# Kernel tuning notes

Hardware: AMD Instinct MI355X
Metric: run time of the kernel (lower is better)

## Reference

```python
import jax, jax.numpy as jnp
import numpy as np

B, N, D_IN, D_OUT, E = 2, 50000, 128, 64, 800000
NEG_SLOPE = 0.2  # LeakyReLU negative slope (alpha)


def setup_inputs() -> dict:
    key = jax.random.key(0)
    ks = jax.random.split(key, 8)
    X_key = jax.random.normal(ks[0], (B, N, D_IN), dtype=jnp.float32)
    X_value = jax.random.normal(ks[1], (B, N, D_IN), dtype=jnp.float32)
    src = jax.random.randint(ks[2], (E,), 0, N, dtype=jnp.int32)
    dst = jnp.sort(jax.random.randint(ks[3], (E,), 0, N, dtype=jnp.int32))
    s = 1.0 / np.sqrt(D_IN)
    Wk = jax.random.normal(ks[4], (D_IN, D_OUT), dtype=jnp.float32) * s
    bk = jnp.zeros((D_OUT,), dtype=jnp.float32)
    Wv = jax.random.normal(ks[5], (D_IN, D_OUT), dtype=jnp.float32) * s
    bv = jnp.zeros((D_OUT,), dtype=jnp.float32)
    return {"X_key": X_key, "X_value": X_value, "Wk": Wk, "bk": bk,
            "Wv": Wv, "bv": bv, "src": src, "dst": dst}


def reference(X_key, X_value, Wk, bk, Wv, bv, src, dst):
    n = X_key.shape[1]
    h_key = X_key @ Wk + bk      # [B, N, D_OUT]
    h_value = X_value @ Wv + bv  # [B, N, D_OUT]

    def per_batch(hk, hv):
        # per-edge dot-product attention score
        e = jnp.sum(hk[src] * hk[dst], axis=-1)                    # [E]
        m = jax.lax.stop_gradient(jax.ops.segment_max(e, dst, num_segments=n))
        a = jnp.exp(e - m[dst])                                    # [E]
        denom = jax.ops.segment_sum(a, dst, num_segments=n)        # [N]
        num = jax.ops.segment_sum(a[:, None] * hv[src], dst, num_segments=n)  # [N, D_OUT]
        # nodes with no incoming edges get 0 (DGL leaves them zero-initialized)
        return num / jnp.where(denom == 0, 1.0, denom)[:, None]

    h_att = jax.vmap(per_batch)(h_key, h_value)  # [B, N, D_OUT]
    # LeakyReLU(alpha=0.2)
    return jnp.where(h_att >= 0, h_att, NEG_SLOPE * h_att)
```

## Files before the change

kernel.cpp:

```cpp
#include <hip/hip_runtime.h>
#include <cfloat>
#include <math.h>

#define D_IN 128
#define D_OUT 64
#define NEG_SLOPE 0.2f
#define ROWH 128
#define SQRT_LOG2E 1.2011224087864498f
#define DEFER_THR 8.0f

typedef _Float16 half2v __attribute__((ext_vector_type(2)));
typedef _Float16 half8 __attribute__((ext_vector_type(8)));
typedef float f32x4 __attribute__((ext_vector_type(4)));

__device__ __forceinline__ unsigned short f2h(float x) {
  union { _Float16 h; unsigned short u; } c;
  c.h = (_Float16)x;
  return c.u;
}
__device__ __forceinline__ float hdot4(unsigned ax, unsigned ay,
                                       unsigned bx, unsigned by) {
  union { unsigned u; half2v h; } al, ah, bl, bh;
  al.u = ax; ah.u = ay; bl.u = bx; bh.u = by;
#if __has_builtin(__builtin_amdgcn_fdot2)
  return __builtin_amdgcn_fdot2(al.h, bl.h,
         __builtin_amdgcn_fdot2(ah.h, bh.h, 0.f, false), false);
#else
  return (float)al.h[0] * (float)bl.h[0] + (float)al.h[1] * (float)bl.h[1] +
         (float)ah.h[0] * (float)bh.h[0] + (float)ah.h[1] * (float)bh.h[1];
#endif
}

__global__ void bfrag_kernel(const float* __restrict__ Wk,
                             const float* __restrict__ Wv,
                             _Float16* __restrict__ bfrag) {
  const int idx = blockIdx.x * 256 + threadIdx.x;
  if (idx >= 2048) return;
  const int which = idx >> 10;
  const float* __restrict__ W = which ? Wv : Wk;
  const float scale = which ? 1.0f : SQRT_LOG2E;
  const int li = idx & 1023;
  const int lane = li & 63;
  const int nt = (li >> 6) & 3;
  const int k0i = li >> 8;
  const int col = nt * 16 + (lane & 15);
  const int kbase = k0i * 32 + (lane >> 4) * 8;
  half8 h;
#pragma unroll
  for (int j = 0; j < 8; ++j)
    h[j] = (_Float16)(W[(size_t)(kbase + j) * D_OUT + col] * scale);
  reinterpret_cast<half8*>(bfrag)[idx] = h;
}

__global__ __launch_bounds__(256) void linear_mfma_kernel(
    const float* __restrict__ Xk, const float* __restrict__ Xv,
    const float* __restrict__ Wk, const float* __restrict__ bk,
    const float* __restrict__ Wv, const float* __restrict__ bv,
    const _Float16* __restrict__ bfrag, unsigned short* __restrict__ hkv,
    int R, int nblk) {
  const int which = (blockIdx.x >= nblk) ? 1 : 0;
  const int blk = blockIdx.x - which * nblk;
  const float* __restrict__ X = which ? Xv : Xk;
  const float* __restrict__ bias = which ? bv : bk;
  const float bscale = which ? 1.0f : SQRT_LOG2E;
  const int uoff = which ? D_OUT : 0;

  const int wave = threadIdx.x >> 6;
  const int lane = threadIdx.x & 63;
  const int r0 = (blk * 4 + wave) * 16;
  if (r0 >= R) return;
  const int rowi = lane & 15;
  const int kgrp = lane >> 4;

  if (r0 + 16 <= R) {
    const half8* btab =
        reinterpret_cast<const half8*>(bfrag) + (which ? 1024 : 0);
    half8 bf[4][4];
#pragma unroll
    for (int k0i = 0; k0i < 4; ++k0i)
#pragma unroll
      for (int nt = 0; nt < 4; ++nt)
        bf[k0i][nt] = btab[(k0i * 4 + nt) * 64 + lane];

    f32x4 acc[4];
#pragma unroll
    for (int nt = 0; nt < 4; ++nt) acc[nt] = (f32x4){0.f, 0.f, 0.f, 0.f};

    const float* xrow = X + (size_t)(r0 + rowi) * D_IN;
#pragma unroll
    for (int k0i = 0; k0i < 4; ++k0i) {
      const float4 x0 =
          *reinterpret_cast<const float4*>(xrow + k0i * 32 + kgrp * 8);
      const float4 x1 =
          *reinterpret_cast<const float4*>(xrow + k0i * 32 + kgrp * 8 + 4);
      half8 a;
      a[0] = (_Float16)x0.x; a[1] = (_Float16)x0.y;
      a[2] = (_Float16)x0.z; a[3] = (_Float16)x0.w;
      a[4] = (_Float16)x1.x; a[5] = (_Float16)x1.y;
      a[6] = (_Float16)x1.z; a[7] = (_Float16)x1.w;
#pragma unroll
      for (int nt = 0; nt < 4; ++nt)
        acc[nt] = __builtin_amdgcn_mfma_f32_16x16x32_f16(a, bf[k0i][nt],
                                                         acc[nt], 0, 0, 0);
    }
#pragma unroll
    for (int nt = 0; nt < 4; ++nt) {
      const int col = nt * 16 + rowi;
      const float bcol = bias[col] * bscale;
#pragma unroll
      for (int r = 0; r < 4; ++r) {
        const int row = r0 + kgrp * 4 + r;
        hkv[(size_t)row * ROWH + uoff + col] = f2h(acc[nt][r] + bcol);
      }
    }
  } else {
    const float* __restrict__ W = which ? Wv : Wk;
    for (int r = r0; r < R; ++r) {
      const float* xr = X + (size_t)r * D_IN;
      float acc = bias[lane];
      for (int k = 0; k < D_IN; ++k)
        acc = fmaf(xr[k], W[(size_t)k * D_OUT + lane], acc);
      acc *= bscale;
      hkv[(size_t)r * ROWH + uoff + lane] = f2h(acc);
    }
  }
}

__global__ void rowptr_kernel(const int* __restrict__ dst, int E, int N,
                              int* __restrict__ row_ptr) {
  int i = blockIdx.x * blockDim.x + threadIdx.x;
  if (i > N) return;
  int lo = 0, hi = E;
  while (lo < hi) {
    int mid = (lo + hi) >> 1;
    if (dst[mid] < i) lo = mid + 1; else hi = mid;
  }
  row_ptr[i] = lo;
}

__device__ __forceinline__ float rowsum16(float p) {
  union { float f; int i; } u, v;
  u.f = p;
  v.i = __builtin_amdgcn_update_dpp(0, u.i, 0x121, 0xF, 0xF, true);
  u.f += v.f;
  v.i = __builtin_amdgcn_update_dpp(0, u.i, 0x122, 0xF, 0xF, true);
  u.f += v.f;
  v.i = __builtin_amdgcn_update_dpp(0, u.i, 0x124, 0xF, 0xF, true);
  u.f += v.f;
  v.i = __builtin_amdgcn_update_dpp(0, u.i, 0x128, 0xF, 0xF, true);
  u.f += v.f;
  return u.f;
}

struct SMState { float m, l; float4 a; };

__device__ __forceinline__ void sm_update(SMState& st, float pl,
                                          const uint2& vu) {
  if (pl > st.m + DEFER_THR) {
    const float sc = exp2f(st.m - pl);
    st.l *= sc;
    st.a.x *= sc; st.a.y *= sc; st.a.z *= sc; st.a.w *= sc;
    st.m = pl;
  }
  const float a = exp2f(pl - st.m);
  union { unsigned u; half2v h; } vlo, vhi;
  vlo.u = vu.x; vhi.u = vu.y;
  st.l += a;
  st.a.x = fmaf(a, (float)vlo.h[0], st.a.x);
  st.a.y = fmaf(a, (float)vlo.h[1], st.a.y);
  st.a.z = fmaf(a, (float)vhi.h[0], st.a.z);
  st.a.w = fmaf(a, (float)vhi.h[1], st.a.w);
}

__device__ __forceinline__ void sm_merge(SMState& d, const SMState& s) {
  const float mn = fmaxf(d.m, s.m);
  const float s1 = exp2f(d.m - mn);
  const float s2 = exp2f(s.m - mn);
  d.l = d.l * s1 + s.l * s2;
  d.a.x = d.a.x * s1 + s.a.x * s2;
  d.a.y = d.a.y * s1 + s.a.y * s2;
  d.a.z = d.a.z * s1 + s.a.z * s2;
  d.a.w = d.a.w * s1 + s.a.w * s2;
  d.m = mn;
}

__device__ __forceinline__ void sm_merge_xor(SMState& d, int off) {
  SMState s;
  s.m = __shfl_xor(d.m, off, 64);
  s.l = __shfl_xor(d.l, off, 64);
  s.a.x = __shfl_xor(d.a.x, off, 64);
  s.a.y = __shfl_xor(d.a.y, off, 64);
  s.a.z = __shfl_xor(d.a.z, off, 64);
  s.a.w = __shfl_xor(d.a.w, off, 64);
  sm_merge(d, s);
}

__device__ __forceinline__ void edge_proc(const char* __restrict__ hb,
                                          unsigned off, const uint2& kd,
                                          SMState& st) {
  const uint2 kq = *reinterpret_cast<const uint2*>(hb + off);
  const uint2 vq = *reinterpret_cast<const uint2*>(hb + off + 128);
  const float pl = rowsum16(hdot4(kq.x, kq.y, kd.x, kd.y));
  sm_update(st, pl, vq);
}

__global__ __launch_bounds__(256) void aggregate_kernel(
    const unsigned short* __restrict__ hkv, const int* __restrict__ src,
    const int* __restrict__ row_ptr, float* __restrict__ out, int N) {
  const int node = blockIdx.x * 4 + (threadIdx.x >> 6);
  const int lane = threadIdx.x & 63;
  if (node >= N) return;
  const char* hb0 = reinterpret_cast<const char*>(hkv);
  const char* hb1 = hb0 + (size_t)N * 256;

  const int li = lane & 15;
  const unsigned li8 = li * 8;
  const int g = lane >> 4;

  const unsigned noff = ((unsigned)node << 8) + li8;
  const uint2 kd0 = *reinterpret_cast<const uint2*>(hb0 + noff);
  const uint2 kd1 = *reinterpret_cast<const uint2*>(hb1 + noff);
  const int e0 = row_ptr[node];
  const int e1 = row_ptr[node + 1];

  SMState A0 = {-FLT_MAX, 0.f, {0.f, 0.f, 0.f, 0.f}};
  SMState B0 = A0, A1 = A0, B1 = A0;

  int e = e0 + g;
  for (; e + 4 < e1; e += 8) {
    const unsigned offA = ((unsigned)src[e] << 8) + li8;
    const unsigned offB = ((unsigned)src[e + 4] << 8) + li8;
    edge_proc(hb0, offA, kd0, A0);
    edge_proc(hb1, offA, kd1, A1);
    edge_proc(hb0, offB, kd0, B0);
    edge_proc(hb1, offB, kd1, B1);
  }
  if (e < e1) {
    const unsigned offA = ((unsigned)src[e] << 8) + li8;
    edge_proc(hb0, offA, kd0, A0);
    edge_proc(hb1, offA, kd1, A1);
  }

  sm_merge(A0, B0);
  sm_merge(A1, B1);
  sm_merge_xor(A0, 16); sm_merge_xor(A0, 32);
  sm_merge_xor(A1, 16); sm_merge_xor(A1, 32);

  if (lane < 16) {
#pragma unroll
    for (int b = 0; b < 2; ++b) {
      const SMState& S = b ? A1 : A0;
      const float denom = (S.l == 0.f) ? 1.f : S.l;
      float4 o;
      o.x = S.a.x / denom; o.y = S.a.y / denom;
      o.z = S.a.z / denom; o.w = S.a.w / denom;
      o.x = (o.x >= 0.f) ? o.x : NEG_SLOPE * o.x;
      o.y = (o.y >= 0.f) ? o.y : NEG_SLOPE * o.y;
      o.z = (o.z >= 0.f) ? o.z : NEG_SLOPE * o.z;
      o.w = (o.w >= 0.f) ? o.w : NEG_SLOPE * o.w;
      *reinterpret_cast<float4*>(out + ((size_t)b * N + node) * D_OUT + 4 * lane) = o;
    }
  }
}

extern "C" void kernel_launch(void* const* d_in, const int* in_sizes, int n_in,
                              void* d_out, int out_size, void* d_ws,
                              size_t ws_size, hipStream_t stream) {
  const float* X_key   = (const float*)d_in[0];
  const float* X_value = (const float*)d_in[1];
  const float* Wk      = (const float*)d_in[2];
  const float* bk      = (const float*)d_in[3];
  const float* Wv      = (const float*)d_in[4];
  const float* bv      = (const float*)d_in[5];
  const int*   src     = (const int*)d_in[6];
  const int*   dst     = (const int*)d_in[7];
  float* out = (float*)d_out;

  const int B = 2;
  const int R = in_sizes[0] / D_IN;
  const int N = R / B;
  const int E = in_sizes[6];

  _Float16* bfrag = (_Float16*)d_ws;
  unsigned short* hkv = (unsigned short*)((char*)d_ws + 32768);
  int* row_ptr = (int*)(hkv + (size_t)R * ROWH);

  const int blocksB = (N + 1 + 255) / 256;
  hipLaunchKernelGGL(rowptr_kernel, dim3(blocksB), dim3(256), 0, stream,
                     dst, E, N, row_ptr);
  hipLaunchKernelGGL(bfrag_kernel, dim3(8), dim3(256), 0, stream,
                     Wk, Wv, bfrag);
  const int wavesPerMat = (R + 15) / 16;
  const int nblk = (wavesPerMat + 3) / 4;
  hipLaunchKernelGGL(linear_mfma_kernel, dim3(2 * nblk), dim3(256), 0, stream,
                     X_key, X_value, Wk, bk, Wv, bv, bfrag, hkv, R, nblk);
  const int blocksC = (N + 3) / 4;
  hipLaunchKernelGGL(aggregate_kernel, dim3(blocksC), dim3(256), 0, stream,
                     hkv, src, row_ptr, out, N);
}
```

Before: 107.3 us.

## Remap aggregate lanes to 8 per batch row with 16-byte loads

Reorganizes the aggregation wavefront so that 8 lanes cover a full 64-wide half-precision row using 16-byte loads, with the two batches split across wave halves instead of each lane processing both batches. Edge groups go from 4 to 4-way unrolled within each batch half, the dot-product reduction uses 3 xor shuffles instead of 4 DPP row adds, and the final merge shrinks. The aim is wider memory transactions, fewer reduction steps and more edges in flight per lane. In exchange each lane carries 8 accumulators, which raises register pressure, and the shuffles may cost more than the DPP ops they replace.

```diff
diff --git a/kernel.cpp b/kernel.cpp
--- a/kernel.cpp
+++ b/kernel.cpp
@@ -18,16 +18,13 @@
   c.h = (_Float16)x;
   return c.u;
 }
-__device__ __forceinline__ float hdot4(unsigned ax, unsigned ay,
-                                       unsigned bx, unsigned by) {
-  union { unsigned u; half2v h; } al, ah, bl, bh;
-  al.u = ax; ah.u = ay; bl.u = bx; bh.u = by;
+__device__ __forceinline__ float hdot2(unsigned a, unsigned b, float c) {
+  union { unsigned u; half2v h; } x, y;
+  x.u = a; y.u = b;
 #if __has_builtin(__builtin_amdgcn_fdot2)
-  return __builtin_amdgcn_fdot2(al.h, bl.h,
-         __builtin_amdgcn_fdot2(ah.h, bh.h, 0.f, false), false);
+  return __builtin_amdgcn_fdot2(x.h, y.h, c, false);
 #else
-  return (float)al.h[0] * (float)bl.h[0] + (float)al.h[1] * (float)bl.h[1] +
-         (float)ah.h[0] * (float)bh.h[0] + (float)ah.h[1] * (float)bh.h[1];
+  return c + (float)x.h[0] * (float)y.h[0] + (float)x.h[1] * (float)y.h[1];
 #endif
 }
 
@@ -138,38 +135,32 @@
   row_ptr[i] = lo;
 }
 
-__device__ __forceinline__ float rowsum16(float p) {
-  union { float f; int i; } u, v;
-  u.f = p;
-  v.i = __builtin_amdgcn_update_dpp(0, u.i, 0x121, 0xF, 0xF, true);
-  u.f += v.f;
-  v.i = __builtin_amdgcn_update_dpp(0, u.i, 0x122, 0xF, 0xF, true);
-  u.f += v.f;
-  v.i = __builtin_amdgcn_update_dpp(0, u.i, 0x124, 0xF, 0xF, true);
-  u.f += v.f;
-  v.i = __builtin_amdgcn_update_dpp(0, u.i, 0x128, 0xF, 0xF, true);
-  u.f += v.f;
-  return u.f;
-}
-
-struct SMState { float m, l; float4 a; };
+struct SMState { float m, l; float4 a0, a1; };
 
 __device__ __forceinline__ void sm_update(SMState& st, float pl,
-                                          const uint2& vu) {
+                                          const uint4& vq) {
   if (pl > st.m + DEFER_THR) {
     const float sc = exp2f(st.m - pl);
     st.l *= sc;
-    st.a.x *= sc; st.a.y *= sc; st.a.z *= sc; st.a.w *= sc;
+    st.a0.x *= sc; st.a0.y *= sc; st.a0.z *= sc; st.a0.w *= sc;
+    st.a1.x *= sc; st.a1.y *= sc; st.a1.z *= sc; st.a1.w *= sc;
     st.m = pl;
   }
   const float a = exp2f(pl - st.m);
-  union { unsigned u; half2v h; } vlo, vhi;
-  vlo.u = vu.x; vhi.u = vu.y;
   st.l += a;
-  st.a.x = fmaf(a, (float)vlo.h[0], st.a.x);
-  st.a.y = fmaf(a, (float)vlo.h[1], st.a.y);
-  st.a.z = fmaf(a, (float)vhi.h[0], st.a.z);
-  st.a.w = fmaf(a, (float)vhi.h[1], st.a.w);
+  union { unsigned u; half2v h; } c;
+  c.u = vq.x;
+  st.a0.x = fmaf(a, (float)c.h[0], st.a0.x);
+  st.a0.y = fmaf(a, (float)c.h[1], st.a0.y);
+  c.u = vq.y;
+  st.a0.z = fmaf(a, (float)c.h[0], st.a0.z);
+  st.a0.w = fmaf(a, (float)c.h[1], st.a0.w);
+  c.u = vq.z;
+  st.a1.x = fmaf(a, (float)c.h[0], st.a1.x);
+  st.a1.y = fmaf(a, (float)c.h[1], st.a1.y);
+  c.u = vq.w;
+  st.a1.z = fmaf(a, (float)c.h[0], st.a1.z);
+  st.a1.w = fmaf(a, (float)c.h[1], st.a1.w);
 }
 
 __device__ __forceinline__ void sm_merge(SMState& d, const SMState& s) {
@@ -177,31 +168,45 @@
   const float s1 = exp2f(d.m - mn);
   const float s2 = exp2f(s.m - mn);
   d.l = d.l * s1 + s.l * s2;
-  d.a.x = d.a.x * s1 + s.a.x * s2;
-  d.a.y = d.a.y * s1 + s.a.y * s2;
-  d.a.z = d.a.z * s1 + s.a.z * s2;
-  d.a.w = d.a.w * s1 + s.a.w * s2;
+  d.a0.x = d.a0.x * s1 + s.a0.x * s2;
+  d.a0.y = d.a0.y * s1 + s.a0.y * s2;
+  d.a0.z = d.a0.z * s1 + s.a0.z * s2;
+  d.a0.w = d.a0.w * s1 + s.a0.w * s2;
+  d.a1.x = d.a1.x * s1 + s.a1.x * s2;
+  d.a1.y = d.a1.y * s1 + s.a1.y * s2;
+  d.a1.z = d.a1.z * s1 + s.a1.z * s2;
+  d.a1.w = d.a1.w * s1 + s.a1.w * s2;
   d.m = mn;
 }
 
-__device__ __forceinline__ void sm_merge_xor(SMState& d, int off) {
+__device__ __forceinline__ void sm_merge_shfl(SMState& d, int off) {
   SMState s;
   s.m = __shfl_xor(d.m, off, 64);
   s.l = __shfl_xor(d.l, off, 64);
-  s.a.x = __shfl_xor(d.a.x, off, 64);
-  s.a.y = __shfl_xor(d.a.y, off, 64);
-  s.a.z = __shfl_xor(d.a.z, off, 64);
-  s.a.w = __shfl_xor(d.a.w, off, 64);
+  s.a0.x = __shfl_xor(d.a0.x, off, 64);
+  s.a0.y = __shfl_xor(d.a0.y, off, 64);
+  s.a0.z = __shfl_xor(d.a0.z, off, 64);
+  s.a0.w = __shfl_xor(d.a0.w, off, 64);
+  s.a1.x = __shfl_xor(d.a1.x, off, 64);
+  s.a1.y = __shfl_xor(d.a1.y, off, 64);
+  s.a1.z = __shfl_xor(d.a1.z, off, 64);
+  s.a1.w = __shfl_xor(d.a1.w, off, 64);
   sm_merge(d, s);
 }
 
-__device__ __forceinline__ void edge_proc(const char* __restrict__ hb,
-                                          unsigned off, const uint2& kd,
+__device__ __forceinline__ void edge_proc(const char* __restrict__ hbase,
+                                          unsigned off, const uint4& kd,
                                           SMState& st) {
-  const uint2 kq = *reinterpret_cast<const uint2*>(hb + off);
-  const uint2 vq = *reinterpret_cast<const uint2*>(hb + off + 128);
-  const float pl = rowsum16(hdot4(kq.x, kq.y, kd.x, kd.y));
-  sm_update(st, pl, vq);
+  const uint4 kq = *reinterpret_cast<const uint4*>(hbase + off);
+  const uint4 vq = *reinterpret_cast<const uint4*>(hbase + off + 128);
+  float p = hdot2(kq.x, kd.x, 0.f);
+  p = hdot2(kq.y, kd.y, p);
+  p = hdot2(kq.z, kd.z, p);
+  p = hdot2(kq.w, kd.w, p);
+  p += __shfl_xor(p, 1, 64);
+  p += __shfl_xor(p, 2, 64);
+  p += __shfl_xor(p, 4, 64);
+  sm_update(st, p, vq);
 }
 
 __global__ __launch_bounds__(256) void aggregate_kernel(
@@ -210,56 +215,62 @@
   const int node = blockIdx.x * 4 + (threadIdx.x >> 6);
   const int lane = threadIdx.x & 63;
   if (node >= N) return;
-  const char* hb0 = reinterpret_cast<const char*>(hkv);
-  const char* hb1 = hb0 + (size_t)N * 256;
-
-  const int li = lane & 15;
-  const unsigned li8 = li * 8;
-  const int g = lane >> 4;
-
-  const unsigned noff = ((unsigned)node << 8) + li8;
-  const uint2 kd0 = *reinterpret_cast<const uint2*>(hb0 + noff);
-  const uint2 kd1 = *reinterpret_cast<const uint2*>(hb1 + noff);
+  const char* hbase = reinterpret_cast<const char*>(hkv);
+
+  const int li = lane & 7;
+  const int w = (lane >> 3) & 3;
+  const int batch = lane >> 5;
+  const unsigned bo = (unsigned)batch * ((unsigned)N * 256u) + (unsigned)li * 16u;
+
+  const uint4 kd =
+      *reinterpret_cast<const uint4*>(hbase + ((unsigned)node << 8) + bo);
   const int e0 = row_ptr[node];
   const int e1 = row_ptr[node + 1];
 
-  SMState A0 = {-FLT_MAX, 0.f, {0.f, 0.f, 0.f, 0.f}};
-  SMState B0 = A0, A1 = A0, B1 = A0;
-
-  int e = e0 + g;
-  for (; e + 4 < e1; e += 8) {
-    const unsigned offA = ((unsigned)src[e] << 8) + li8;
-    const unsigned offB = ((unsigned)src[e + 4] << 8) + li8;
-    edge_proc(hb0, offA, kd0, A0);
-    edge_proc(hb1, offA, kd1, A1);
-    edge_proc(hb0, offB, kd0, B0);
-    edge_proc(hb1, offB, kd1, B1);
-  }
-  if (e < e1) {
-    const unsigned offA = ((unsigned)src[e] << 8) + li8;
-    edge_proc(hb0, offA, kd0, A0);
-    edge_proc(hb1, offA, kd1, A1);
-  }
-
-  sm_merge(A0, B0);
-  sm_merge(A1, B1);
-  sm_merge_xor(A0, 16); sm_merge_xor(A0, 32);
-  sm_merge_xor(A1, 16); sm_merge_xor(A1, 32);
-
-  if (lane < 16) {
-#pragma unroll
-    for (int b = 0; b < 2; ++b) {
-      const SMState& S = b ? A1 : A0;
-      const float denom = (S.l == 0.f) ? 1.f : S.l;
-      float4 o;
-      o.x = S.a.x / denom; o.y = S.a.y / denom;
-      o.z = S.a.z / denom; o.w = S.a.w / denom;
-      o.x = (o.x >= 0.f) ? o.x : NEG_SLOPE * o.x;
-      o.y = (o.y >= 0.f) ? o.y : NEG_SLOPE * o.y;
-      o.z = (o.z >= 0.f) ? o.z : NEG_SLOPE * o.z;
-      o.w = (o.w >= 0.f) ? o.w : NEG_SLOPE * o.w;
-      *reinterpret_cast<float4*>(out + ((size_t)b * N + node) * D_OUT + 4 * lane) = o;
-    }
+  SMState A = {-FLT_MAX, 0.f, {0, 0, 0, 0}, {0, 0, 0, 0}};
+  SMState B = A, C = A, D = A;
+
+  int e = e0 + w;
+  for (; e + 12 < e1; e += 16) {
+    const unsigned oA = ((unsigned)src[e] << 8) + bo;
+    const unsigned oB = ((unsigned)src[e + 4] << 8) + bo;
+    const unsigned oC = ((unsigned)src[e + 8] << 8) + bo;
+    const unsigned oD = ((unsigned)src[e + 12] << 8) + bo;
+    edge_proc(hbase, oA, kd, A);
+    edge_proc(hbase, oB, kd, B);
+    edge_proc(hbase, oC, kd, C);
+    edge_proc(hbase, oD, kd, D);
+  }
+  for (; e < e1; e += 4) {
+    const unsigned oA = ((unsigned)src[e] << 8) + bo;
+    edge_proc(hbase, oA, kd, A);
+  }
+
+  sm_merge(A, B);
+  sm_merge(C, D);
+  sm_merge(A, C);
+  sm_merge_shfl(A, 8);
+  sm_merge_shfl(A, 16);
+
+  if (w == 0) {
+    const float denom = (A.l == 0.f) ? 1.f : A.l;
+    const float inv = 1.f / denom;
+    float4 o0, o1;
+    o0.x = A.a0.x * inv; o0.y = A.a0.y * inv;
+    o0.z = A.a0.z * inv; o0.w = A.a0.w * inv;
+    o1.x = A.a1.x * inv; o1.y = A.a1.y * inv;
+    o1.z = A.a1.z * inv; o1.w = A.a1.w * inv;
+    o0.x = (o0.x >= 0.f) ? o0.x : NEG_SLOPE * o0.x;
+    o0.y = (o0.y >= 0.f) ? o0.y : NEG_SLOPE * o0.y;
+    o0.z = (o0.z >= 0.f) ? o0.z : NEG_SLOPE * o0.z;
+    o0.w = (o0.w >= 0.f) ? o0.w : NEG_SLOPE * o0.w;
+    o1.x = (o1.x >= 0.f) ? o1.x : NEG_SLOPE * o1.x;
+    o1.y = (o1.y >= 0.f) ? o1.y : NEG_SLOPE * o1.y;
+    o1.z = (o1.z >= 0.f) ? o1.z : NEG_SLOPE * o1.z;
+    o1.w = (o1.w >= 0.f) ? o1.w : NEG_SLOPE * o1.w;
+    float* orow = out + ((size_t)batch * N + node) * D_OUT + li * 8;
+    reinterpret_cast<float4*>(orow)[0] = o0;
+    reinterpret_cast<float4*>(orow)[1] = o1;
   }
 }
 
```

New measurement: 110.4 us. 2.9% more time.
